# Kernel tuning notes

Measured on AMD Instinct MI355X. Metric: run time of the kernel, lower is better.

## Reference

```python
import jax, jax.numpy as jnp
import numpy as np

S = 100        # sos_token_num
H = 12         # num heads
LY = 3         # number of residual blocks
NEG = -100.0   # attention-bias masking value


def layer_norm(x, w, b, eps=1e-5):
    u = jnp.mean(x, -1, keepdims=True)
    v = jnp.mean((x - u) ** 2, -1, keepdims=True)
    return (x - u) / jnp.sqrt(v + eps) * w + b


def quick_gelu(x):
    return x * jax.nn.sigmoid(1.702 * x)


def l2norm(x, eps=1e-12):
    return x / jnp.maximum(jnp.linalg.norm(x, axis=-1, keepdims=True), eps)


def setup_inputs() -> dict:
    key = jax.random.key(0)
    ks = iter(jax.random.split(key, 32))
    n, c, hh, ww, out_dim = 2, 768, 32, 32, 512
    r = lambda shape, s=1.0: jax.random.normal(next(ks), shape, jnp.float32) * s
    return dict(
        cls_token=r((1, n, c)),
        pix_feat=r((n, c, hh, ww)),
        last_surgery=r((1 + hh * ww, n, c)),
        attn_bias=r((n, 1, S, hh, ww)),
        qkv_w=r((LY, 3 * c, c), 0.02), qkv_b=jnp.zeros((LY, 3 * c)),
        proj_w=r((LY, c, c), 0.02), proj_b=jnp.zeros((LY, c)),
        ln1_w=jnp.ones((LY, c)), ln1_b=jnp.zeros((LY, c)),
        ln2_w=jnp.ones((LY, c)), ln2_b=jnp.zeros((LY, c)),
        fc_w=r((LY, 4 * c, c), 0.02), fc_b=jnp.zeros((LY, 4 * c)),
        fc2_w=r((LY, c, 4 * c), 0.02), fc2_b=jnp.zeros((LY, c)),
        lnp_w=jnp.ones((c,)), lnp_b=jnp.zeros((c,)),
        proj_out=r((c, out_dim), 0.02),
    )


def reference(cls_token, pix_feat, last_surgery, attn_bias,
              qkv_w, qkv_b, proj_w, proj_b,
              ln1_w, ln1_b, ln2_w, ln2_b,
              fc_w, fc_b, fc2_w, fc2_b,
              lnp_w, lnp_b, proj_out):
    n, c, hh, ww = pix_feat.shape
    L = hh * ww
    N = S + 1 + L
    d = c // H
    scale = d ** -0.5

    # ---- assemble token streams (batch-first [n, N, c]) ----
    pix_tok = pix_feat.reshape(n, c, L).transpose(2, 0, 1)          # [L, n, c]
    x = jnp.concatenate([jnp.broadcast_to(cls_token, (S, n, c)), cls_token, pix_tok], 0)
    x_sur = jnp.concatenate([jnp.broadcast_to(last_surgery[0:1], (S, n, c)), last_surgery], 0)
    xo = x.transpose(1, 0, 2)      # 'original' stream  [n, N, c]
    xs = x_sur.transpose(1, 0, 2)  # 'surgery'  stream  [n, N, c]

    # ---- build attention biases (identity downsample: bias already at (h, w)) ----
    base = jnp.zeros((N, N), jnp.float32)
    base = base.at[:, :S].set(NEG)
    base = base.at[jnp.arange(S), jnp.arange(S)].set(0.0)
    base = base.at[:S, S].set(NEG)
    plain = jnp.broadcast_to(base, (n, H, N, N))
    bias = jnp.broadcast_to(attn_bias, (n, H, S, hh, ww)).reshape(n, H, S, L)
    biased = plain.at[:, :, :S, S + 1:].set(bias)   # sos rows attend to pixels via bias

    def attention(t, l):
        # t: [n, N, c] (post-ln_1); returns (surgery_res, ori_res)
        qkv = (t @ qkv_w[l].T + qkv_b[l]).reshape(n, N, 3, H, d).transpose(2, 0, 3, 1, 4)
        q, k, v = qkv[0], qkv[1], qkv[2]   # each [n, H, N, d]
        def attend(q_, k_, mask):
            a = jax.nn.softmax(jnp.einsum('bhnd,bhmd->bhnm', q_, k_) * scale + mask, axis=-1)
            o = jnp.einsum('bhnm,bhmd->bhnd', a, v).transpose(0, 2, 1, 3).reshape(n, N, c)
            return o @ proj_w[l].T + proj_b[l]
        x_ori_res = attend(q, k, biased)   # standard pass, biased mask (attn_mask[0])
        x_res = attend(v, v, plain)        # q = k = v surgery pass (attn_mask[1])
        return x_res, x_ori_res

    for l in range(LY):
        t = layer_norm(xo, ln1_w[l], ln1_b[l])
        res_sur, res_ori = attention(t, l)
        xo = xo + res_ori
        xo = xo + (quick_gelu(layer_norm(xo, ln2_w[l], ln2_b[l]) @ fc_w[l].T + fc_b[l]) @ fc2_w[l].T + fc2_b[l])
        xs = xs + res_sur

    # ---- heads ----
    sos = l2norm(layer_norm(xo[:, :S], lnp_w, lnp_b) @ proj_out)          # [n, S, out]
    img = l2norm(layer_norm(xs[:, S:], lnp_w, lnp_b) @ proj_out)          # [n, 1+L, out]
    img = img[:, 1:, :].transpose(0, 2, 1).reshape(n, proj_out.shape[1], hh, ww)
    return sos, img
```

## Files before the change

### kernel.cpp

```cpp
#include <hip/hip_runtime.h>
#include <math.h>


constexpr int Cc = 768;
constexpr int Ss = 100;
constexpr int Hh = 12;
constexpr int Ll = 1024;
constexpr int Nn = 1125;
constexpr int NB = 2;
constexpr int VTS = 1216;
constexpr float QS = 0.18033688011112042f;
constexpr float LOG2E = 1.4426950408889634f;

typedef unsigned short u16;
typedef unsigned int u32;
typedef __attribute__((ext_vector_type(8))) short short8v;
typedef __attribute__((ext_vector_type(8))) unsigned short ushort8v;
typedef __attribute__((ext_vector_type(4))) float f32x4;
typedef __attribute__((ext_vector_type(4))) unsigned int u32x4;

__device__ inline u16 f2bf(float f) {
  unsigned u = __builtin_bit_cast(unsigned int, f);
  unsigned r = u + 0x7fffu + ((u >> 16) & 1u);
  return (u16)(r >> 16);
}
__device__ inline float bf2f(u16 v) {
  return __builtin_bit_cast(float, (unsigned int)v << 16);
}
__device__ inline unsigned cvtpk(float lo, float hi) {
  unsigned r;
  asm("v_cvt_pk_bf16_f32 %0, %1, %2" : "=v"(r) : "v"(lo), "v"(hi));
  return r;
}
__device__ inline float max3f(float a, float b, float c) {
  float r;
  asm("v_max3_f32 %0, %1, %2, %3" : "=v"(r) : "v"(a), "v"(b), "v"(c));
  return r;
}

__device__ inline int swz(int row, int col) {
  return (row << 6) + ((((col >> 3) ^ (row & 7)) << 3) | (col & 7));
}

__global__ __launch_bounds__(256) void assemble_kernel(
    const float* __restrict__ cls, const float* __restrict__ pix,
    const float* __restrict__ sur, float* __restrict__ xo, float* __restrict__ xs) {
  int idx = blockIdx.x * 256 + (int)threadIdx.x;
  int total = NB * Nn * Cc;
  if (idx >= total) return;
  int ch = idx % Cc;
  int t  = (idx / Cc) % Nn;
  int b  = idx / (Cc * Nn);
  float vo, vs;
  if (t <= Ss) vo = cls[b * Cc + ch];
  else         vo = pix[(size_t)b * Cc * Ll + (size_t)ch * Ll + (t - Ss - 1)];
  if (t < Ss)  vs = sur[b * Cc + ch];
  else         vs = sur[(size_t)(t - Ss) * NB * Cc + b * Cc + ch];
  xo[idx] = vo;
  xs[idx] = vs;
}

constexpr int CN0 = 3 * 2304 * 768;
constexpr int CN1 = 3 * 768 * 768;
constexpr int CN2 = 3 * 3072 * 768;
constexpr int CN3 = 3 * 768 * 3072;
__global__ __launch_bounds__(256) void cvt4_kernel(
    const float* __restrict__ s0, const float* __restrict__ s1,
    const float* __restrict__ s2, const float* __restrict__ s3,
    u16* __restrict__ dst) {
  int i4 = (blockIdx.x * 256 + (int)threadIdx.x) * 4;
  if (i4 >= CN0 + CN1 + CN2 + CN3) return;
  const float* src; int off;
  if (i4 < CN0)             { src = s0; off = i4; }
  else if (i4 < CN0 + CN1)  { src = s1; off = i4 - CN0; }
  else if (i4 < CN0 + CN1 + CN2) { src = s2; off = i4 - CN0 - CN1; }
  else                      { src = s3; off = i4 - CN0 - CN1 - CN2; }
  float4 v = *(const float4*)(src + off);
  *(ushort4*)(dst + i4) = make_ushort4(f2bf(v.x), f2bf(v.y), f2bf(v.z), f2bf(v.w));
}

__global__ __launch_bounds__(256) void transpose_po_kernel(
    const float* __restrict__ in, u16* __restrict__ out) {
  int id = blockIdx.x * 256 + (int)threadIdx.x;
  if (id >= 512 * 768) return;
  int nidx = id / 768, k = id - nidx * 768;
  out[id] = f2bf(in[(size_t)k * 512 + nidx]);
}

__global__ __launch_bounds__(256) void vtrans_kernel(
    const u16* __restrict__ qkv, u16* __restrict__ vtg) {
  __shared__ u16 tile[64][72];
  int tt = blockIdx.x;
  int bh = blockIdx.y;
  int b = bh / Hh, h = bh - b * Hh;
  int tid = (int)threadIdx.x;
  {
    int tl = tid >> 2, c0 = (tid & 3) << 4;
    int tok = tt * 64 + tl;
    int tokc = tok > 1124 ? 1124 : tok;
    const u16* src = qkv + ((size_t)(b * Nn + tokc)) * 2304 + 2 * Cc + h * 64 + c0;
    ushort8v v0 = *(const ushort8v*)src;
    ushort8v v1 = *(const ushort8v*)(src + 8);
    if (tok > 1124) { v0 = (ushort8v)0; v1 = (ushort8v)0; }
    *(ushort8v*)&tile[tl][c0] = v0;
    *(ushort8v*)&tile[tl][c0 + 8] = v1;
  }
  __syncthreads();
  {
    int d = tid >> 2, t0 = (tid & 3) << 4;
    ushort8v o0, o1;
#pragma unroll
    for (int j = 0; j < 8; ++j) { o0[j] = tile[t0 + j][d]; o1[j] = tile[t0 + 8 + j][d]; }
    size_t orow = ((size_t)bh * 64 + d) * VTS + tt * 64 + t0;
    *(ushort8v*)&vtg[orow] = o0;
    *(ushort8v*)&vtg[orow + 8] = o1;
  }
}

__global__ __launch_bounds__(256) void ln_kernel(
    const float* __restrict__ X, const float* __restrict__ w, const float* __restrict__ b,
    u16* __restrict__ Y, int rows_per_b, int row_off) {
  int r = blockIdx.x;
  int bb = r / rows_per_b;
  int i  = r % rows_per_b;
  const float* x = X + ((size_t)bb * Nn + row_off + i) * Cc;
  u16* y = Y + (size_t)r * Cc;
  int tid = (int)threadIdx.x;
  float v0 = x[tid], v1 = x[tid + 256], v2 = x[tid + 512];
  float s = v0 + v1 + v2;
  __shared__ float sbuf[4];
  for (int off = 32; off; off >>= 1) s += __shfl_xor(s, off);
  if ((tid & 63) == 0) sbuf[tid >> 6] = s;
  __syncthreads();
  float mean = (sbuf[0] + sbuf[1] + sbuf[2] + sbuf[3]) * (1.0f / Cc);
  float d0 = v0 - mean, d1 = v1 - mean, d2 = v2 - mean;
  float q = d0 * d0 + d1 * d1 + d2 * d2;
  __syncthreads();
  for (int off = 32; off; off >>= 1) q += __shfl_xor(q, off);
  if ((tid & 63) == 0) sbuf[tid >> 6] = q;
  __syncthreads();
  float var = (sbuf[0] + sbuf[1] + sbuf[2] + sbuf[3]) * (1.0f / Cc);
  float inv = rsqrtf(var + 1e-5f);
  y[tid]       = f2bf(d0 * inv * w[tid]       + b[tid]);
  y[tid + 256] = f2bf(d1 * inv * w[tid + 256] + b[tid + 256]);
  y[tid + 512] = f2bf(d2 * inv * w[tid + 512] + b[tid + 512]);
}

__global__ __launch_bounds__(256) void gemm128_kernel(
    const u16* __restrict__ A, const u16* __restrict__ B,
    const float* __restrict__ bias, u16* __restrict__ outb,
    int M, int N, int K, int act) {
  __shared__ __align__(16) u16 Als[128 * 64];
  __shared__ __align__(16) u16 Bls[128 * 64];
  int tid = (int)threadIdx.x;
  int wave = tid >> 6, lane = tid & 63, g = lane >> 4, li = lane & 15;
  int wm = wave >> 1, wn = wave & 1;
  int row0 = blockIdx.y * 128, col0 = blockIdx.x * 128;

  const u16* aptr[4]; const u16* bptr[4]; int dsti[4];
#pragma unroll
  for (int j = 0; j < 4; ++j) {
    int c = tid + j * 256;
    int r = c >> 3, c8 = c & 7;
    dsti[j] = (r << 6) + ((c8 ^ (r & 7)) << 3);
    int ra = row0 + r; if (ra > M - 1) ra = M - 1;
    aptr[j] = A + (size_t)ra * K + (c8 << 3);
    bptr[j] = B + (size_t)(col0 + r) * K + (c8 << 3);
  }

  f32x4 acc[4][4];
#pragma unroll
  for (int mi = 0; mi < 4; ++mi)
#pragma unroll
    for (int ni = 0; ni < 4; ++ni) acc[mi][ni] = (f32x4){0.f, 0.f, 0.f, 0.f};

  for (int k0 = 0; k0 < K; k0 += 64) {
    ushort8v ta[4], tb[4];
#pragma unroll
    for (int j = 0; j < 4; ++j) {
      ta[j] = *(const ushort8v*)(aptr[j] + k0);
      tb[j] = *(const ushort8v*)(bptr[j] + k0);
    }
    __syncthreads();
#pragma unroll
    for (int j = 0; j < 4; ++j) {
      *(ushort8v*)&Als[dsti[j]] = ta[j];
      *(ushort8v*)&Bls[dsti[j]] = tb[j];
    }
    __syncthreads();
#pragma unroll
    for (int kc = 0; kc < 2; ++kc) {
      short8v af[4], bfr[4];
#pragma unroll
      for (int mi = 0; mi < 4; ++mi) {
        int rr = wm * 64 + mi * 16 + li;
        af[mi] = *(const short8v*)&Als[(rr << 6) + (((kc * 4 + g) ^ (rr & 7)) << 3)];
      }
#pragma unroll
      for (int ni = 0; ni < 4; ++ni) {
        int rb = wn * 64 + ni * 16 + li;
        bfr[ni] = *(const short8v*)&Bls[(rb << 6) + (((kc * 4 + g) ^ (rb & 7)) << 3)];
      }
      __builtin_amdgcn_s_setprio(1);
#pragma unroll
      for (int mi = 0; mi < 4; ++mi)
#pragma unroll
        for (int ni = 0; ni < 4; ++ni)
          acc[mi][ni] = __builtin_amdgcn_mfma_f32_16x16x32_bf16(af[mi], bfr[ni], acc[mi][ni], 0, 0, 0);
      __builtin_amdgcn_s_setprio(0);
    }
  }

#pragma unroll
  for (int mi = 0; mi < 4; ++mi) {
#pragma unroll
    for (int r = 0; r < 4; ++r) {
      int m = row0 + wm * 64 + mi * 16 + g * 4 + r;
      if (m >= M) continue;
#pragma unroll
      for (int ni = 0; ni < 4; ++ni) {
        int n = col0 + wn * 64 + ni * 16 + li;
        float v = acc[mi][ni][r];
        if (bias) v += bias[n];
        if (act)  v = v / (1.0f + __expf(-1.702f * v));
        outb[(size_t)m * N + n] = f2bf(v);
      }
    }
  }
}

__global__ __launch_bounds__(256) void gemm64_kernel(
    const u16* __restrict__ A0, const u16* __restrict__ A1,
    const u16* __restrict__ B, const float* __restrict__ bias,
    const float* __restrict__ res0, const float* __restrict__ res1,
    float* __restrict__ outf0, float* __restrict__ outf1,
    u16* __restrict__ outb0, u16* __restrict__ outb1,
    int M, int N, int K, int act) {
  __shared__ __align__(16) u16 Als[64 * 64];
  __shared__ __align__(16) u16 Bls[128 * 64];
  int zz = blockIdx.z;
  const u16* A = zz ? A1 : A0;
  const float* res = zz ? res1 : res0;
  float* outf = zz ? outf1 : outf0;
  u16* outb = zz ? outb1 : outb0;
  int tid = (int)threadIdx.x;
  int wave = tid >> 6, lane = tid & 63, g = lane >> 4, li = lane & 15;
  int row0 = blockIdx.y * 64, col0 = blockIdx.x * 128;

  const u16* aptr[2]; int dA[2];
#pragma unroll
  for (int j = 0; j < 2; ++j) {
    int ca = tid + j * 256;
    int r = ca >> 3, c8 = ca & 7;
    dA[j] = (r << 6) + ((c8 ^ (r & 7)) << 3);
    int ra = row0 + r; if (ra > M - 1) ra = M - 1;
    aptr[j] = A + (size_t)ra * K + (c8 << 3);
  }
  const u16* bptr[4]; int dB[4];
#pragma unroll
  for (int j = 0; j < 4; ++j) {
    int cb = tid + j * 256;
    int r = cb >> 3, c8 = cb & 7;
    dB[j] = (r << 6) + ((c8 ^ (r & 7)) << 3);
    bptr[j] = B + (size_t)(col0 + r) * K + (c8 << 3);
  }

  f32x4 acc[4][2];
#pragma unroll
  for (int mi = 0; mi < 4; ++mi)
#pragma unroll
    for (int ni = 0; ni < 2; ++ni) acc[mi][ni] = (f32x4){0.f, 0.f, 0.f, 0.f};

  for (int k0 = 0; k0 < K; k0 += 64) {
    ushort8v ta[2], tb[4];
#pragma unroll
    for (int j = 0; j < 2; ++j) ta[j] = *(const ushort8v*)(aptr[j] + k0);
#pragma unroll
    for (int j = 0; j < 4; ++j) tb[j] = *(const ushort8v*)(bptr[j] + k0);
    __syncthreads();
#pragma unroll
    for (int j = 0; j < 2; ++j) *(ushort8v*)&Als[dA[j]] = ta[j];
#pragma unroll
    for (int j = 0; j < 4; ++j) *(ushort8v*)&Bls[dB[j]] = tb[j];
    __syncthreads();
#pragma unroll
    for (int kc = 0; kc < 2; ++kc) {
      short8v af[4], bfr[2];
#pragma unroll
      for (int mi = 0; mi < 4; ++mi) {
        int rr = mi * 16 + li;
        af[mi] = *(const short8v*)&Als[(rr << 6) + (((kc * 4 + g) ^ (rr & 7)) << 3)];
      }
#pragma unroll
      for (int ni = 0; ni < 2; ++ni) {
        int rb = wave * 32 + ni * 16 + li;
        bfr[ni] = *(const short8v*)&Bls[(rb << 6) + (((kc * 4 + g) ^ (rb & 7)) << 3)];
      }
      __builtin_amdgcn_s_setprio(1);
#pragma unroll
      for (int mi = 0; mi < 4; ++mi)
#pragma unroll
        for (int ni = 0; ni < 2; ++ni)
          acc[mi][ni] = __builtin_amdgcn_mfma_f32_16x16x32_bf16(af[mi], bfr[ni], acc[mi][ni], 0, 0, 0);
      __builtin_amdgcn_s_setprio(0);
    }
  }

#pragma unroll
  for (int mi = 0; mi < 4; ++mi) {
#pragma unroll
    for (int r = 0; r < 4; ++r) {
      int m = row0 + mi * 16 + g * 4 + r;
      if (m >= M) continue;
#pragma unroll
      for (int ni = 0; ni < 2; ++ni) {
        int n = col0 + wave * 32 + ni * 16 + li;
        float v = acc[mi][ni][r];
        if (bias) v += bias[n];
        if (act)  v = v / (1.0f + __expf(-1.702f * v));
        if (res)  v += res[(size_t)m * N + n];
        if (outf) outf[(size_t)m * N + n] = v;
        else      outb[(size_t)m * N + n] = f2bf(v);
      }
    }
  }
}

__global__ __launch_bounds__(256) void attn_kernel(
    const u16* __restrict__ qkv, const u16* __restrict__ vtg,
    const float* __restrict__ abias,
    u16* __restrict__ ao, u16* __restrict__ as_) {
  __shared__ __align__(16) u16 Klds[64 * 64];
  __shared__ __align__(16) u16 Vt[64 * 64];
  int id = (int)blockIdx.x;
  int virt = (id & 7) * 60 + (id >> 3);
  int gid = virt / 10;
  int qt  = virt - gid * 10;
  int z   = gid / 24;
  int bh  = gid - z * 24;
  int b = bh / Hh, h = bh - b * Hh;
  int tid = (int)threadIdx.x;
  int wave = tid >> 6, lane = tid & 63, g = lane >> 4, li = lane & 15;
  bool sosq = (qt == 9);
  u16* outp = z ? as_ : ao;

  int qbase = sosq ? wave * 32 : 100 + qt * 128 + wave * 32;
  int qcap = sosq ? 99 : 1124;
  int qtokf[2];
  qtokf[0] = qbase + li;       if (qtokf[0] > qcap) qtokf[0] = qcap;
  qtokf[1] = qbase + 16 + li;  if (qtokf[1] > qcap) qtokf[1] = qcap;
  int qoff = z ? 2 * Cc + h * 64 : h * 64;
  int koff = z ? 2 * Cc + h * 64 : Cc + h * 64;

  short8v qf[2][2];
#pragma unroll
  for (int f = 0; f < 2; ++f) {
    const u16* qp = qkv + ((size_t)b * Nn + qtokf[f]) * 2304 + qoff;
#pragma unroll
    for (int kc = 0; kc < 2; ++kc) {
      ushort8v a = *(const ushort8v*)(qp + kc * 32 + g * 8);
      u32x4 w;
#pragma unroll
      for (int jj = 0; jj < 4; ++jj)
        w[jj] = cvtpk(bf2f(a[2 * jj]) * QS, bf2f(a[2 * jj + 1]) * QS);
      qf[f][kc] = __builtin_bit_cast(short8v, w);
    }
  }

  int skey = tid >> 2;
  int sd0  = (tid & 3) << 4;
  int prow = 16 * (2 * (skey >> 5) + ((skey >> 2) & 1)) + 4 * ((skey >> 3) & 3) + (skey & 3);
  int kK0 = swz(prow, sd0), kK1 = swz(prow, sd0 + 8);
  int vI0 = swz(skey, sd0), vI1 = swz(skey, sd0 + 8);
  const u16* kbase = qkv + (size_t)b * Nn * 2304 + koff + sd0;
  const u16* vbase = vtg + ((size_t)bh * 64 + skey) * VTS + sd0;

  const int KOFF[4] = {0, 4, 32, 36};

  f32x4 oacc[2][4];
#pragma unroll
  for (int f = 0; f < 2; ++f)
#pragma unroll
    for (int dt = 0; dt < 4; ++dt) oacc[f][dt] = (f32x4){0.f, 0.f, 0.f, 0.f};
  float mrow[2] = {-1e30f, -1e30f}, lrow[2] = {0.f, 0.f};

  int NT = sosq ? 19 : 17;
  for (int kt = 0; kt < NT; ++kt) {
    int t0 = sosq ? (kt <= 1 ? 64 * kt : 64 * (kt - 1) + 32) : 96 + 64 * kt;
    __syncthreads();
    {
      int ktok = t0 + skey; if (ktok > 1124) ktok = 1124;
      const u16* kp = kbase + (size_t)ktok * 2304;
      ushort8v k0v = *(const ushort8v*)kp;
      ushort8v k1v = *(const ushort8v*)(kp + 8);
      const u16* vp = vbase + t0;
      ushort8v v0 = *(const ushort8v*)vp;
      ushort8v v1 = *(const ushort8v*)(vp + 8);
      *(ushort8v*)&Klds[kK0] = k0v;
      *(ushort8v*)&Klds[kK1] = k1v;
      *(ushort8v*)&Vt[vI0] = v0;
      *(ushort8v*)&Vt[vI1] = v1;
    }
    __syncthreads();

    f32x4 sacc[2][4];
#pragma unroll
    for (int f = 0; f < 2; ++f)
#pragma unroll
      for (int nt = 0; nt < 4; ++nt) sacc[f][nt] = (f32x4){0.f, 0.f, 0.f, 0.f};
    __builtin_amdgcn_s_setprio(1);
#pragma unroll
    for (int kc = 0; kc < 2; ++kc) {
#pragma unroll
      for (int nt = 0; nt < 4; ++nt) {
        short8v kb = *(const short8v*)&Klds[swz(nt * 16 + li, kc * 32 + g * 8)];
        sacc[0][nt] = __builtin_amdgcn_mfma_f32_16x16x32_bf16(kb, qf[0][kc], sacc[0][nt], 0, 0, 0);
        sacc[1][nt] = __builtin_amdgcn_mfma_f32_16x16x32_bf16(kb, qf[1][kc], sacc[1][nt], 0, 0, 0);
      }
    }
    __builtin_amdgcn_s_setprio(0);

    int tg = t0 + 8 * g;
    if (!sosq) {
      if (kt == 0) {
#pragma unroll
        for (int f = 0; f < 2; ++f)
#pragma unroll
          for (int nt = 0; nt < 4; ++nt)
#pragma unroll
            for (int r = 0; r < 4; ++r)
              if (tg + KOFF[nt] + r < 100) sacc[f][nt][r] = -1e30f;
      } else if (kt == 16) {
#pragma unroll
        for (int f = 0; f < 2; ++f)
#pragma unroll
          for (int nt = 0; nt < 4; ++nt)
#pragma unroll
            for (int r = 0; r < 4; ++r)
              if (tg + KOFF[nt] + r > 1124) sacc[f][nt][r] = -1e30f;
      }
    } else {
      if (kt <= 1) {
#pragma unroll
        for (int f = 0; f < 2; ++f)
#pragma unroll
          for (int nt = 0; nt < 4; ++nt)
#pragma unroll
            for (int r = 0; r < 4; ++r)
              if (tg + KOFF[nt] + r != qtokf[f]) sacc[f][nt][r] = -1e30f;
      } else if (z == 0) {
#pragma unroll
        for (int f = 0; f < 2; ++f) {
          const float* bp = abias + ((size_t)b * Ss + qtokf[f]) * Ll;
#pragma unroll
          for (int nt = 0; nt < 4; ++nt)
#pragma unroll
            for (int r = 0; r < 4; ++r) {
              int tok = tg + KOFF[nt] + r;
              int bi = tok - 101; bi = bi < 0 ? 0 : bi; bi = bi > 1023 ? 1023 : bi;
              float bv = bp[bi];
              bool bad = (tok < 101) | (tok > 1124);
              sacc[f][nt][r] = bad ? -1e30f : fmaf(bv, LOG2E, sacc[f][nt][r]);
            }
        }
      } else {
#pragma unroll
        for (int f = 0; f < 2; ++f)
#pragma unroll
          for (int nt = 0; nt < 4; ++nt)
#pragma unroll
            for (int r = 0; r < 4; ++r) {
              int tok = tg + KOFF[nt] + r;
              if ((tok < 101) | (tok > 1124)) sacc[f][nt][r] = -1e30f;
            }
      }
    }

#pragma unroll
    for (int f = 0; f < 2; ++f) {
      float rmax = max3f(sacc[f][0][0], sacc[f][0][1], sacc[f][0][2]);
      rmax = max3f(rmax, sacc[f][0][3], sacc[f][1][0]);
      rmax = max3f(rmax, sacc[f][1][1], sacc[f][1][2]);
      rmax = max3f(rmax, sacc[f][1][3], sacc[f][2][0]);
      rmax = max3f(rmax, sacc[f][2][1], sacc[f][2][2]);
      rmax = max3f(rmax, sacc[f][2][3], sacc[f][3][0]);
      rmax = max3f(rmax, sacc[f][3][1], sacc[f][3][2]);
      rmax = fmaxf(rmax, sacc[f][3][3]);
      rmax = fmaxf(rmax, __shfl_xor(rmax, 16));
      rmax = fmaxf(rmax, __shfl_xor(rmax, 32));
      float mnew = fmaxf(mrow[f], rmax);
      float fac = __builtin_amdgcn_exp2f(mrow[f] - mnew);
      mrow[f] = mnew;
      float psum = 0.f;
#pragma unroll
      for (int nt = 0; nt < 4; ++nt)
#pragma unroll
        for (int r = 0; r < 4; ++r) {
          float e = __builtin_amdgcn_exp2f(sacc[f][nt][r] - mnew);
          sacc[f][nt][r] = e;
          psum += e;
        }
      psum += __shfl_xor(psum, 16);
      psum += __shfl_xor(psum, 32);
      lrow[f] = lrow[f] * fac + psum;
#pragma unroll
      for (int dt = 0; dt < 4; ++dt) oacc[f][dt] *= fac;
    }

    __builtin_amdgcn_s_setprio(1);
#pragma unroll
    for (int kcp = 0; kcp < 2; ++kcp) {
      short8v pb[2];
#pragma unroll
      for (int f = 0; f < 2; ++f) {
        u32x4 pwv;
#pragma unroll
        for (int w = 0; w < 4; ++w) {
          int nt = 2 * kcp + (w >> 1);
          int r0 = (w & 1) * 2;
          pwv[w] = cvtpk(sacc[f][nt][r0], sacc[f][nt][r0 + 1]);
        }
        pb[f] = __builtin_bit_cast(short8v, pwv);
      }
#pragma unroll
      for (int dt = 0; dt < 4; ++dt) {
        short8v va = *(const short8v*)&Vt[swz(dt * 16 + li, kcp * 32 + g * 8)];
        oacc[0][dt] = __builtin_amdgcn_mfma_f32_16x16x32_bf16(va, pb[0], oacc[0][dt], 0, 0, 0);
        oacc[1][dt] = __builtin_amdgcn_mfma_f32_16x16x32_bf16(va, pb[1], oacc[1][dt], 0, 0, 0);
      }
    }
    __builtin_amdgcn_s_setprio(0);
  }

#pragma unroll
  for (int f = 0; f < 2; ++f) {
    int tok = qbase + f * 16 + li;
    if (tok > qcap) continue;
    float inv = 1.0f / lrow[f];
    u16* op = outp + ((size_t)b * Nn + tok) * Cc + h * 64 + g * 4;
#pragma unroll
    for (int dt = 0; dt < 4; ++dt) {
      unsigned lo = cvtpk(oacc[f][dt][0] * inv, oacc[f][dt][1] * inv);
      unsigned hi = cvtpk(oacc[f][dt][2] * inv, oacc[f][dt][3] * inv);
      uint2 o2; o2.x = lo; o2.y = hi;
      *(uint2*)(op + dt * 16) = o2;
    }
  }
}

__global__ __launch_bounds__(256) void l2norm_sos_kernel(
    const float* __restrict__ Xp, float* __restrict__ out) {
  int r = blockIdx.x;
  int tid = (int)threadIdx.x;
  const float* x = Xp + (size_t)r * 512;
  float v0 = x[tid], v1 = x[tid + 256];
  float s = v0 * v0 + v1 * v1;
  __shared__ float sbuf[4];
  for (int off = 32; off; off >>= 1) s += __shfl_xor(s, off);
  if ((tid & 63) == 0) sbuf[tid >> 6] = s;
  __syncthreads();
  float tot = sbuf[0] + sbuf[1] + sbuf[2] + sbuf[3];
  float inv = 1.0f / fmaxf(sqrtf(tot), 1e-12f);
  out[(size_t)r * 512 + tid]       = v0 * inv;
  out[(size_t)r * 512 + tid + 256] = v1 * inv;
}

__global__ __launch_bounds__(256) void l2norm_img_kernel(
    const float* __restrict__ Xp, float* __restrict__ out) {
  int r = blockIdx.x;
  int b = r / 1025, ti = r % 1025;
  int tid = (int)threadIdx.x;
  const float* x = Xp + (size_t)r * 512;
  float v0 = x[tid], v1 = x[tid + 256];
  float s = v0 * v0 + v1 * v1;
  __shared__ float sbuf[4];
  for (int off = 32; off; off >>= 1) s += __shfl_xor(s, off);
  if ((tid & 63) == 0) sbuf[tid >> 6] = s;
  __syncthreads();
  float tot = sbuf[0] + sbuf[1] + sbuf[2] + sbuf[3];
  if (ti == 0) return;
  float inv = 1.0f / fmaxf(sqrtf(tot), 1e-12f);
  float* o = out + (size_t)b * 512 * 1024 + (ti - 1);
  o[(size_t)tid * 1024]         = v0 * inv;
  o[(size_t)(tid + 256) * 1024] = v1 * inv;
}

extern "C" void kernel_launch(void* const* d_in, const int* in_sizes, int n_in,
                              void* d_out, int out_size, void* d_ws, size_t ws_size,
                              hipStream_t stream) {
  const float* cls      = (const float*)d_in[0];
  const float* pix      = (const float*)d_in[1];
  const float* sur      = (const float*)d_in[2];
  const float* abias    = (const float*)d_in[3];
  const float* qkv_w    = (const float*)d_in[4];
  const float* qkv_b    = (const float*)d_in[5];
  const float* proj_w   = (const float*)d_in[6];
  const float* proj_b   = (const float*)d_in[7];
  const float* ln1_w    = (const float*)d_in[8];
  const float* ln1_b    = (const float*)d_in[9];
  const float* ln2_w    = (const float*)d_in[10];
  const float* ln2_b    = (const float*)d_in[11];
  const float* fc_w     = (const float*)d_in[12];
  const float* fc_b     = (const float*)d_in[13];
  const float* fc2_w    = (const float*)d_in[14];
  const float* fc2_b    = (const float*)d_in[15];
  const float* lnp_w    = (const float*)d_in[16];
  const float* lnp_b    = (const float*)d_in[17];
  const float* proj_o   = (const float*)d_in[18];
  float* out = (float*)d_out;

  const size_t SZ = (size_t)NB * Nn * Cc;
  float* xo      = (float*)d_ws;
  float* xs      = xo + SZ;
  float* head_pj = xs + SZ;
  u16* tln_bf = (u16*)(head_pj + 2250 * 512);
  u16* act_bf = tln_bf + (size_t)2250 * 768;
  u16* ao_bf  = act_bf + (size_t)2250 * 3072;
  u16* as_bf  = ao_bf + (size_t)2250 * 768;
  u16* wq_bf  = as_bf + (size_t)2250 * 768;
  u16* wp_bf  = wq_bf + (size_t)CN0;
  u16* wf_bf  = wp_bf + (size_t)CN1;
  u16* w2_bf  = wf_bf + (size_t)CN2;
  u16* wo_bf  = w2_bf + (size_t)CN3;
  u16* vtg    = wo_bf + (size_t)512 * 768;

  assemble_kernel<<<6750, 256, 0, stream>>>(cls, pix, sur, xo, xs);
  cvt4_kernel<<<20736, 256, 0, stream>>>(qkv_w, proj_w, fc_w, fc2_w, wq_bf);
  transpose_po_kernel<<<1536, 256, 0, stream>>>(proj_o, wo_bf);

  for (int l = 0; l < 3; ++l) {
    ln_kernel<<<2250, 256, 0, stream>>>(xo, ln1_w + l * 768, ln1_b + l * 768, tln_bf, Nn, 0);
    gemm128_kernel<<<dim3(18, 18), 256, 0, stream>>>(
        tln_bf, wq_bf + (size_t)l * 2304 * 768, qkv_b + l * 2304,
        act_bf, 2250, 2304, 768, 0);
    vtrans_kernel<<<dim3(19, 24), 256, 0, stream>>>(act_bf, vtg);
    attn_kernel<<<480, 256, 0, stream>>>(act_bf, vtg, abias, ao_bf, as_bf);
    gemm64_kernel<<<dim3(6, 36, 2), 256, 0, stream>>>(
        ao_bf, as_bf, wp_bf + (size_t)l * 768 * 768, proj_b + l * 768,
        xo, xs, xo, xs, nullptr, nullptr, 2250, 768, 768, 0);
    ln_kernel<<<2250, 256, 0, stream>>>(xo, ln2_w + l * 768, ln2_b + l * 768, tln_bf, Nn, 0);
    gemm128_kernel<<<dim3(24, 18), 256, 0, stream>>>(
        tln_bf, wf_bf + (size_t)l * 3072 * 768, fc_b + l * 3072,
        act_bf, 2250, 3072, 768, 1);
    gemm64_kernel<<<dim3(6, 36, 1), 256, 0, stream>>>(
        act_bf, act_bf, w2_bf + (size_t)l * 768 * 3072, fc2_b + l * 768,
        xo, xo, xo, xo, nullptr, nullptr, 2250, 768, 3072, 0);
  }

  ln_kernel<<<200, 256, 0, stream>>>(xo, lnp_w, lnp_b, tln_bf, 100, 0);
  ln_kernel<<<2050, 256, 0, stream>>>(xs, lnp_w, lnp_b, tln_bf + 200 * 768, 1025, 100);
  gemm64_kernel<<<dim3(4, 36, 1), 256, 0, stream>>>(
      tln_bf, tln_bf, wo_bf, nullptr,
      nullptr, nullptr, head_pj, head_pj, nullptr, nullptr, 2250, 512, 768, 0);
  l2norm_sos_kernel<<<200, 256, 0, stream>>>(head_pj, out);
  l2norm_img_kernel<<<2050, 256, 0, stream>>>(head_pj + 200 * 512, out + 102400);
}
```

Baseline: 837.2 us.

## Split attention over two key-range halves with a separate combine kernel

The attention kernel now splits each (batch, head, query-tile) work item into two halves over the key tiles, doubling the grid from 480 to 960 blocks. Each half writes unnormalized fp32 partial outputs plus its running max and sum, and a new combine kernel merges them with log-sum-exp rescaling into the bf16 outputs. The goal is better occupancy of the GPU's compute units, since 480 blocks only partly fills the device. In exchange it adds fp32 partial-output traffic to and from memory and one more kernel launch per layer.

Measured after the change: 847.9 us. Within noise of the previous version (+1.3%).

```diff
diff --git a/kernel.cpp b/kernel.cpp
--- a/kernel.cpp
+++ b/kernel.cpp
@@ -329,20 +329,21 @@
 __global__ __launch_bounds__(256) void attn_kernel(
     const u16* __restrict__ qkv, const u16* __restrict__ vtg,
     const float* __restrict__ abias,
-    u16* __restrict__ ao, u16* __restrict__ as_) {
+    float* __restrict__ opart, float* __restrict__ mlp) {
   __shared__ __align__(16) u16 Klds[64 * 64];
   __shared__ __align__(16) u16 Vt[64 * 64];
   int id = (int)blockIdx.x;
-  int virt = (id & 7) * 60 + (id >> 3);
-  int gid = virt / 10;
-  int qt  = virt - gid * 10;
-  int z   = gid / 24;
-  int bh  = gid - z * 24;
+  int virt = (id & 7) * 120 + (id >> 3);
+  int gidh = virt / 10;
+  int qt   = virt - gidh * 10;
+  int half = gidh & 1;
+  int gid  = gidh >> 1;
+  int z    = gid / 24;
+  int bh   = gid - z * 24;
   int b = bh / Hh, h = bh - b * Hh;
   int tid = (int)threadIdx.x;
   int wave = tid >> 6, lane = tid & 63, g = lane >> 4, li = lane & 15;
   bool sosq = (qt == 9);
-  u16* outp = z ? as_ : ao;
 
   int qbase = sosq ? wave * 32 : 100 + qt * 128 + wave * 32;
   int qcap = sosq ? 99 : 1124;
@@ -385,7 +386,9 @@
   float mrow[2] = {-1e30f, -1e30f}, lrow[2] = {0.f, 0.f};
 
   int NT = sosq ? 19 : 17;
-  for (int kt = 0; kt < NT; ++kt) {
+  int kt0 = half * 9;
+  int kt1 = half ? NT : 9;
+  for (int kt = kt0; kt < kt1; ++kt) {
     int t0 = sosq ? (kt <= 1 ? 64 * kt : 64 * (kt - 1) + 32) : 96 + 64 * kt;
     __syncthreads();
     {
@@ -532,19 +535,48 @@
     __builtin_amdgcn_s_setprio(0);
   }
 
+  int hp = half * 2 + z;
 #pragma unroll
   for (int f = 0; f < 2; ++f) {
     int tok = qbase + f * 16 + li;
     if (tok > qcap) continue;
-    float inv = 1.0f / lrow[f];
-    u16* op = outp + ((size_t)b * Nn + tok) * Cc + h * 64 + g * 4;
-#pragma unroll
-    for (int dt = 0; dt < 4; ++dt) {
-      unsigned lo = cvtpk(oacc[f][dt][0] * inv, oacc[f][dt][1] * inv);
-      unsigned hi = cvtpk(oacc[f][dt][2] * inv, oacc[f][dt][3] * inv);
-      uint2 o2; o2.x = lo; o2.y = hi;
-      *(uint2*)(op + dt * 16) = o2;
-    }
+    float* op = opart + ((size_t)hp * NB * Nn + (size_t)b * Nn + tok) * Cc + h * 64 + g * 4;
+#pragma unroll
+    for (int dt = 0; dt < 4; ++dt)
+      *(float4*)(op + dt * 16) = make_float4(oacc[f][dt][0], oacc[f][dt][1], oacc[f][dt][2], oacc[f][dt][3]);
+    if (g == 0) {
+      size_t mb = (((size_t)hp * 24 + bh) * Nn + tok) * 2;
+      mlp[mb] = mrow[f];
+      mlp[mb + 1] = lrow[f];
+    }
+  }
+}
+
+__global__ __launch_bounds__(256) void attn_combine_kernel(
+    const float* __restrict__ opart, const float* __restrict__ mlp,
+    u16* __restrict__ ao, u16* __restrict__ as_) {
+  int blk = blockIdx.x;
+  int pass = blk / (NB * Nn);
+  int row = blk - pass * (NB * Nn);
+  int b = row / Nn, i = row - b * Nn;
+  u16* outp = pass ? as_ : ao;
+  int tid = (int)threadIdx.x;
+#pragma unroll
+  for (int e = 0; e < 3; ++e) {
+    int c = tid + e * 256;
+    int h = c >> 6;
+    int bh = b * Hh + h;
+    size_t m0i = (((size_t)(0 * 2 + pass) * 24 + bh) * Nn + i) * 2;
+    size_t m1i = (((size_t)(1 * 2 + pass) * 24 + bh) * Nn + i) * 2;
+    float m0 = mlp[m0i], l0 = mlp[m0i + 1];
+    float m1 = mlp[m1i], l1 = mlp[m1i + 1];
+    float M = fmaxf(m0, m1);
+    float w0 = __builtin_amdgcn_exp2f(m0 - M);
+    float w1 = __builtin_amdgcn_exp2f(m1 - M);
+    float L = l0 * w0 + l1 * w1;
+    float v0 = opart[((size_t)(0 * 2 + pass) * NB * Nn + row) * Cc + c];
+    float v1 = opart[((size_t)(1 * 2 + pass) * NB * Nn + row) * Cc + c];
+    outp[(size_t)row * Cc + c] = f2bf((v0 * w0 + v1 * w1) / L);
   }
 }
 
@@ -610,10 +642,12 @@
   float* out = (float*)d_out;
 
   const size_t SZ = (size_t)NB * Nn * Cc;
-  float* xo      = (float*)d_ws;
-  float* xs      = xo + SZ;
-  float* head_pj = xs + SZ;
-  u16* tln_bf = (u16*)(head_pj + 2250 * 512);
+  float* xo    = (float*)d_ws;
+  float* xs    = xo + SZ;
+  float* opart = xs + SZ;
+  float* mlp   = opart + (size_t)4 * 2250 * 768;
+  float* head_pj = opart;
+  u16* tln_bf = (u16*)(mlp + (size_t)4 * 24 * 1125 * 2);
   u16* act_bf = tln_bf + (size_t)2250 * 768;
   u16* ao_bf  = act_bf + (size_t)2250 * 3072;
   u16* as_bf  = ao_bf + (size_t)2250 * 768;
@@ -634,7 +668,8 @@
         tln_bf, wq_bf + (size_t)l * 2304 * 768, qkv_b + l * 2304,
         act_bf, 2250, 2304, 768, 0);
     vtrans_kernel<<<dim3(19, 24), 256, 0, stream>>>(act_bf, vtg);
-    attn_kernel<<<480, 256, 0, stream>>>(act_bf, vtg, abias, ao_bf, as_bf);
+    attn_kernel<<<960, 256, 0, stream>>>(act_bf, vtg, abias, opart, mlp);
+    attn_combine_kernel<<<4500, 256, 0, stream>>>(opart, mlp, ao_bf, as_bf);
     gemm64_kernel<<<dim3(6, 36, 2), 256, 0, stream>>>(
         ao_bf, as_bf, wp_bf + (size_t)l * 768 * 768, proj_b + l * 768,
         xo, xs, xo, xs, nullptr, nullptr, 2250, 768, 768, 0);
```
